# Kernel tuning notes

Hardware: AMD Instinct MI355X
Metric: run time of the kernel (lower is better)

Reference implementation:

```python
import jax, jax.numpy as jnp
import numpy as np

B, T, C = 2, 2048, 2048
N_HEAD, N_KV = 16, 2
D_HEAD = C // N_HEAD          # 128
R = N_HEAD // N_KV            # q heads per kv head = 8


def setup_inputs() -> dict:
    key = jax.random.key(0)
    ks = jax.random.split(key, 5)
    s = 0.02
    return {
        "x": jax.random.normal(ks[0], (B, T, C), dtype=jnp.float32),
        "Wq": jax.random.normal(ks[1], (C, C), dtype=jnp.float32) * s,
        "Wk": jax.random.normal(ks[2], (C, N_KV * D_HEAD), dtype=jnp.float32) * s,
        "Wv": jax.random.normal(ks[3], (C, N_KV * D_HEAD), dtype=jnp.float32) * s,
        "Wo": jax.random.normal(ks[4], (C, C), dtype=jnp.float32) * s,
    }


def reference(x, Wq, Wk, Wv, Wo):
    b, t, c = x.shape
    # projections (no bias per config.bias=False)
    q = (x @ Wq).reshape(b, t, N_KV, R, D_HEAD)        # group q heads by kv group
    k = (x @ Wk).reshape(b, t, N_KV, D_HEAD)
    v = (x @ Wv).reshape(b, t, N_KV, D_HEAD)
    scale = 1.0 / jnp.sqrt(jnp.float32(D_HEAD))
    # scores: [b, g(kv), r, tq, tk] -- broadcast kv heads instead of repeat_interleave
    att = jnp.einsum('btgrd,bsgd->bgrts', q, k) * scale
    causal = jnp.tril(jnp.ones((t, t), dtype=bool))
    att = jnp.where(causal, att, -jnp.inf)
    att = jax.nn.softmax(att, axis=-1)
    y = jnp.einsum('bgrts,bsgd->btgrd', att, v).reshape(b, t, c)
    return y @ Wo
```

## Files before the change

kernel.cpp:

```cpp
#include <hip/hip_runtime.h>
#include <stdint.h>

using bf16x8 = __attribute__((ext_vector_type(8))) __bf16;
using f32x4  = __attribute__((ext_vector_type(4))) float;

#define GLL(g, l) __builtin_amdgcn_global_load_lds(                                  \
    (const __attribute__((address_space(1))) void*)(g),                              \
    (__attribute__((address_space(3))) void*)(l), 16, 0, 0)

__device__ __forceinline__ unsigned short f2bf(float f) {
  unsigned u = __builtin_bit_cast(unsigned, f);
  u += 0x7FFF + ((u >> 16) & 1);
  return (unsigned short)(u >> 16);
}

__global__ __launch_bounds__(256) void cast_kernel(const float* __restrict__ in,
                                                   unsigned short* __restrict__ out, int n4) {
  int i = blockIdx.x * 256 + threadIdx.x;
  if (i >= n4) return;
  float4 v = reinterpret_cast<const float4*>(in)[i];
  ushort4 o;
  o.x = f2bf(v.x); o.y = f2bf(v.y); o.z = f2bf(v.z); o.w = f2bf(v.w);
  reinterpret_cast<ushort4*>(out)[i] = o;
}

__global__ __launch_bounds__(256) void tcast_kernel(const float* __restrict__ W,
                                                    unsigned short* __restrict__ Wt,
                                                    int K, int N) {
  __shared__ float T[64][65];
  const int k0 = blockIdx.x * 64, n0 = blockIdx.y * 64;
  const int t = threadIdx.x;
  const int r4 = t >> 6, c = t & 63;
#pragma unroll
  for (int p = 0; p < 16; ++p) {
    int r = p * 4 + r4;
    T[r][c] = W[(size_t)(k0 + r) * N + n0 + c];
  }
  __syncthreads();
#pragma unroll
  for (int p = 0; p < 16; ++p) {
    int r = p * 4 + r4;
    Wt[(size_t)(n0 + r) * K + k0 + c] = f2bf(T[c][r]);
  }
}

__global__ __launch_bounds__(256) void tv_kernel(const unsigned short* __restrict__ V,
                                                 unsigned short* __restrict__ Vt) {
  __shared__ unsigned short T[64][68];
  const int t0 = blockIdx.x * 64;
  const int d0 = blockIdx.y * 64;
  const int t = threadIdx.x;
  const int r4 = t >> 6, c = t & 63;
#pragma unroll
  for (int p = 0; p < 16; ++p) {
    int r = p * 4 + r4;
    T[r][c] = V[(size_t)(t0 + r) * 2560 + 2304 + d0 + c];
  }
  __syncthreads();
  const int b = t0 >> 11;
  const int tl = t0 & 2047;
#pragma unroll
  for (int p = 0; p < 16; ++p) {
    int dr = p * 4 + r4;
    int dg = d0 + dr;
    int g = dg >> 7, dl = dg & 127;
    Vt[(size_t)((b * 2 + g) * 128 + dl) * 2048 + tl + c] = T[c][dr];
  }
}

template <bool FP32OUT>
__global__ __launch_bounds__(256) void gemm_bt_kernel(const unsigned short* __restrict__ A,
                                                      const unsigned short* __restrict__ Bt,
                                                      void* __restrict__ Cout,
                                                      int K, int lda, int ldb, int ldc,
                                                      float scale, int nscale) {
  __shared__ __align__(16) unsigned short As[128 * 64];
  __shared__ __align__(16) unsigned short Bs[128 * 64];
  const int m0 = blockIdx.x * 128, n0 = blockIdx.y * 128;
  const int t = threadIdx.x;
  const int w = t >> 6, lane = t & 63;
  const int l15 = lane & 15, quad = lane >> 4;
  const int wm = (w >> 1) * 64, wn = (w & 1) * 64;

  const int srow = lane >> 3;
  const int sgl = (lane & 7) ^ srow;

  f32x4 acc[4][4] = {};

  for (int k0 = 0; k0 < K; k0 += 64) {
    __syncthreads();
#pragma unroll
    for (int p = 0; p < 4; ++p) {
      int rowbase = p * 32 + w * 8;
      GLL(&A[(size_t)(m0 + rowbase + srow) * lda + k0 + sgl * 8], &As[rowbase * 64]);
      GLL(&Bt[(size_t)(n0 + rowbase + srow) * ldb + k0 + sgl * 8], &Bs[rowbase * 64]);
    }
    __syncthreads();
#pragma unroll
    for (int kk = 0; kk < 64; kk += 32) {
      const int kg = kk >> 3;
      const int phys = ((kg + quad) ^ (l15 & 7)) * 8;
      bf16x8 af[4], bfr[4];
#pragma unroll
      for (int mt = 0; mt < 4; ++mt)
        af[mt] = *reinterpret_cast<const bf16x8*>(&As[(wm + mt * 16 + l15) * 64 + phys]);
#pragma unroll
      for (int nt = 0; nt < 4; ++nt)
        bfr[nt] = *reinterpret_cast<const bf16x8*>(&Bs[(wn + nt * 16 + l15) * 64 + phys]);
#pragma unroll
      for (int mt = 0; mt < 4; ++mt)
#pragma unroll
        for (int nt = 0; nt < 4; ++nt)
          acc[mt][nt] = __builtin_amdgcn_mfma_f32_16x16x32_bf16(af[mt], bfr[nt], acc[mt][nt], 0, 0, 0);
    }
  }

  const float sc = (n0 < nscale) ? scale : 1.0f;
#pragma unroll
  for (int mt = 0; mt < 4; ++mt) {
#pragma unroll
    for (int reg = 0; reg < 4; ++reg) {
      int row = m0 + wm + mt * 16 + quad * 4 + reg;
#pragma unroll
      for (int nt = 0; nt < 4; ++nt) {
        int col = n0 + wn + nt * 16 + l15;
        float v = acc[mt][nt][reg] * sc;
        if (FP32OUT)
          reinterpret_cast<float*>(Cout)[(size_t)row * ldc + col] = v;
        else
          reinterpret_cast<unsigned short*>(Cout)[(size_t)row * ldc + col] = f2bf(v);
      }
    }
  }
}

#define LDQK 2560
__global__ __launch_bounds__(256) void attn_kernel(const unsigned short* __restrict__ Q,
                                                   const unsigned short* __restrict__ Kg,
                                                   const unsigned short* __restrict__ Vt,
                                                   unsigned short* __restrict__ Y) {
  __shared__ __align__(16) unsigned short Ks[64 * 128];
  __shared__ __align__(16) unsigned short Vs[128 * 64];
  __shared__ __align__(16) unsigned short Ps[4][32 * 68];

  const int iq = blockIdx.x;
  const int hh = blockIdx.y & 15;
  const int b  = blockIdx.y >> 4;
  const int g  = hh >> 3;
  const int t = threadIdx.x;
  const int w = t >> 6, lane = t & 63;
  const int l15 = lane & 15, quad = lane >> 4;

  bf16x8 qf[2][4];
#pragma unroll
  for (int mi = 0; mi < 2; ++mi) {
    int qrow = iq * 128 + w * 32 + mi * 16 + l15;
    const unsigned short* qp = &Q[(size_t)(b * 2048 + qrow) * LDQK + hh * 128 + quad * 8];
#pragma unroll
    for (int dk = 0; dk < 4; ++dk)
      qf[mi][dk] = *reinterpret_cast<const bf16x8*>(qp + dk * 32);
  }

  f32x4 o[2][8] = {};
  float l_run[2][4] = {};

  const int k_r = lane >> 4;
  const int v_r = lane >> 3;

  const int nkt = 2 * iq + 2;
  for (int kt = 0; kt < nkt; ++kt) {
    __syncthreads();
#pragma unroll
    for (int p = 0; p < 4; ++p) {
      int rowbase = p * 16 + w * 4;
      int row = rowbase + k_r;
      int gl = (lane & 15) ^ (row & 15);
      GLL(&Kg[(size_t)(b * 2048 + kt * 64 + row) * LDQK + g * 128 + gl * 8], &Ks[rowbase * 128]);
    }
#pragma unroll
    for (int p = 0; p < 4; ++p) {
      int rowbase = p * 32 + w * 8;
      int row = rowbase + v_r;
      int gl = (lane & 7) ^ (row & 7);
      GLL(&Vt[(size_t)((b * 2 + g) * 128 + row) * 2048 + kt * 64 + gl * 8], &Vs[rowbase * 64]);
    }
    __syncthreads();

#pragma unroll
    for (int mi = 0; mi < 2; ++mi) {
      f32x4 s[4];
#pragma unroll
      for (int nt = 0; nt < 4; ++nt) {
        f32x4 a = {};
#pragma unroll
        for (int dk = 0; dk < 4; ++dk) {
          int phys = (dk * 4 + quad) ^ l15;
          bf16x8 kf = *reinterpret_cast<const bf16x8*>(&Ks[(nt * 16 + l15) * 128 + phys * 8]);
          a = __builtin_amdgcn_mfma_f32_16x16x32_bf16(qf[mi][dk], kf, a, 0, 0, 0);
        }
        s[nt] = a;
      }
      if (kt >= 2 * iq) {
#pragma unroll
        for (int nt = 0; nt < 4; ++nt) {
          int kcol = kt * 64 + nt * 16 + l15;
#pragma unroll
          for (int reg = 0; reg < 4; ++reg) {
            int qr = iq * 128 + w * 32 + mi * 16 + quad * 4 + reg;
            if (kcol > qr) s[nt][reg] = -1e30f;
          }
        }
      }
#pragma unroll
      for (int nt = 0; nt < 4; ++nt) {
#pragma unroll
        for (int reg = 0; reg < 4; ++reg) {
          float p = __builtin_exp2f(__builtin_fmaf(s[nt][reg], 1.44269504f, -23.08312064f));
          l_run[mi][reg] += p;
          Ps[w][(mi * 16 + quad * 4 + reg) * 68 + nt * 16 + l15] = f2bf(p);
        }
      }
    }

#pragma unroll
    for (int kk = 0; kk < 2; ++kk) {
      const int kg = kk * 4;
      bf16x8 pf[2];
#pragma unroll
      for (int mi = 0; mi < 2; ++mi)
        pf[mi] = *reinterpret_cast<const bf16x8*>(&Ps[w][(mi * 16 + l15) * 68 + kk * 32 + quad * 8]);
#pragma unroll
      for (int dt = 0; dt < 8; ++dt) {
        int phys = (kg + quad) ^ (l15 & 7);
        bf16x8 vf = *reinterpret_cast<const bf16x8*>(&Vs[(dt * 16 + l15) * 64 + phys * 8]);
#pragma unroll
        for (int mi = 0; mi < 2; ++mi)
          o[mi][dt] = __builtin_amdgcn_mfma_f32_16x16x32_bf16(pf[mi], vf, o[mi][dt], 0, 0, 0);
      }
    }
  }

#pragma unroll
  for (int off = 1; off <= 8; off <<= 1)
#pragma unroll
    for (int mi = 0; mi < 2; ++mi)
#pragma unroll
      for (int reg = 0; reg < 4; ++reg)
        l_run[mi][reg] += __shfl_xor(l_run[mi][reg], off);
  float inv[2][4];
#pragma unroll
  for (int mi = 0; mi < 2; ++mi)
#pragma unroll
    for (int reg = 0; reg < 4; ++reg) inv[mi][reg] = 1.0f / l_run[mi][reg];

#pragma unroll
  for (int mi = 0; mi < 2; ++mi)
#pragma unroll
    for (int dt = 0; dt < 8; ++dt)
#pragma unroll
      for (int reg = 0; reg < 4; ++reg) {
        int row = b * 2048 + iq * 128 + w * 32 + mi * 16 + quad * 4 + reg;
        int col = hh * 128 + dt * 16 + l15;
        Y[(size_t)row * 2048 + col] = f2bf(o[mi][dt][reg] * inv[mi][reg]);
      }
}

extern "C" void kernel_launch(void* const* d_in, const int* in_sizes, int n_in,
                              void* d_out, int out_size, void* d_ws, size_t ws_size,
                              hipStream_t stream) {
  const float* x  = (const float*)d_in[0];
  const float* Wq = (const float*)d_in[1];
  const float* Wk = (const float*)d_in[2];
  const float* Wv = (const float*)d_in[3];
  const float* Wo = (const float*)d_in[4];

  char* ws = (char*)d_ws;
  unsigned short* xb    = (unsigned short*)(ws + 0);
  unsigned short* Wqkvt = (unsigned short*)(ws + 16777216);
  unsigned short* Wot   = (unsigned short*)(ws + 27262976);
  unsigned short* QKVb  = (unsigned short*)(ws + 35651584);
  unsigned short* Vtb   = (unsigned short*)(ws + 56623104);
  unsigned short* Yb    = xb;

  cast_kernel<<<8192, 256, 0, stream>>>(x, xb, 2097152);
  tcast_kernel<<<dim3(32, 32), 256, 0, stream>>>(Wq, Wqkvt, 2048, 2048);
  tcast_kernel<<<dim3(32, 4),  256, 0, stream>>>(Wk, Wqkvt + (size_t)2048 * 2048, 2048, 256);
  tcast_kernel<<<dim3(32, 4),  256, 0, stream>>>(Wv, Wqkvt + (size_t)2304 * 2048, 2048, 256);
  tcast_kernel<<<dim3(32, 32), 256, 0, stream>>>(Wo, Wot, 2048, 2048);

  const float qscale = 0.08838834764831845f;
  gemm_bt_kernel<false><<<dim3(32, 20), 256, 0, stream>>>(xb, Wqkvt, QKVb,
                                                          2048, 2048, 2048, 2560, qscale, 2048);
  tv_kernel<<<dim3(64, 4), 256, 0, stream>>>(QKVb, Vtb);
  attn_kernel<<<dim3(16, 32), 256, 0, stream>>>(QKVb, QKVb + 2048, Vtb, Yb);
  gemm_bt_kernel<true><<<dim3(32, 16), 256, 0, stream>>>(Yb, Wot, d_out,
                                                         2048, 2048, 2048, 2048, 1.0f, 0);
}
```

Before: 324.5 us.

## Pair causal query tiles per block and prefetch K/V via registers

Each attention block now processes two query tiles (iq and 15-iq) to balance causal work, halving the grid. K/V tiles are prefetched one iteration ahead into registers and then stored to LDS, replacing direct global-to-LDS loads. The QK^T loop computes both row groups together to reuse K fragments. This trades lower occupancy (one block per CU, higher register use) for balanced work and overlapped loads.

After: 354.4 us. +9.2%, slower.

```diff
diff --git a/kernel.cpp b/kernel.cpp
--- a/kernel.cpp
+++ b/kernel.cpp
@@ -135,15 +135,15 @@
 }
 
 #define LDQK 2560
-__global__ __launch_bounds__(256) void attn_kernel(const unsigned short* __restrict__ Q,
-                                                   const unsigned short* __restrict__ Kg,
-                                                   const unsigned short* __restrict__ Vt,
-                                                   unsigned short* __restrict__ Y) {
+__global__ __launch_bounds__(256, 1) void attn_kernel(const unsigned short* __restrict__ Q,
+                                                      const unsigned short* __restrict__ Kg,
+                                                      const unsigned short* __restrict__ Vt,
+                                                      unsigned short* __restrict__ Y) {
   __shared__ __align__(16) unsigned short Ks[64 * 128];
   __shared__ __align__(16) unsigned short Vs[128 * 64];
   __shared__ __align__(16) unsigned short Ps[4][32 * 68];
 
-  const int iq = blockIdx.x;
+  const int bx = blockIdx.x;
   const int hh = blockIdx.y & 15;
   const int b  = blockIdx.y >> 4;
   const int g  = hh >> 3;
@@ -151,118 +151,141 @@
   const int w = t >> 6, lane = t & 63;
   const int l15 = lane & 15, quad = lane >> 4;
 
-  bf16x8 qf[2][4];
-#pragma unroll
-  for (int mi = 0; mi < 2; ++mi) {
-    int qrow = iq * 128 + w * 32 + mi * 16 + l15;
-    const unsigned short* qp = &Q[(size_t)(b * 2048 + qrow) * LDQK + hh * 128 + quad * 8];
-#pragma unroll
-    for (int dk = 0; dk < 4; ++dk)
-      qf[mi][dk] = *reinterpret_cast<const bf16x8*>(qp + dk * 32);
-  }
-
-  f32x4 o[2][8] = {};
-  float l_run[2][4] = {};
-
-  const int k_r = lane >> 4;
-  const int v_r = lane >> 3;
-
-  const int nkt = 2 * iq + 2;
-  for (int kt = 0; kt < nkt; ++kt) {
-    __syncthreads();
-#pragma unroll
-    for (int p = 0; p < 4; ++p) {
-      int rowbase = p * 16 + w * 4;
-      int row = rowbase + k_r;
-      int gl = (lane & 15) ^ (row & 15);
-      GLL(&Kg[(size_t)(b * 2048 + kt * 64 + row) * LDQK + g * 128 + gl * 8], &Ks[rowbase * 128]);
-    }
-#pragma unroll
-    for (int p = 0; p < 4; ++p) {
-      int rowbase = p * 32 + w * 8;
-      int row = rowbase + v_r;
-      int gl = (lane & 7) ^ (row & 7);
-      GLL(&Vt[(size_t)((b * 2 + g) * 128 + row) * 2048 + kt * 64 + gl * 8], &Vs[rowbase * 64]);
-    }
-    __syncthreads();
-
+  const unsigned short* Kbase = Kg + (size_t)b * 2048 * LDQK + g * 128;
+  const unsigned short* Vbase = Vt + (size_t)(b * 2 + g) * 128 * 2048;
+
+  const int krow = t >> 4;
+  const int kgl  = (t & 15);
+  const int vrow = t >> 3;
+  const int vgl  = (t & 7);
+
+  int4 kst[4], vst[4];
+#pragma unroll
+  for (int p = 0; p < 4; ++p) {
+    int rk = p * 16 + krow;
+    kst[p] = *reinterpret_cast<const int4*>(&Kbase[(size_t)rk * LDQK + ((kgl ^ (rk & 15)) * 8)]);
+    int rv = p * 32 + vrow;
+    vst[p] = *reinterpret_cast<const int4*>(&Vbase[(size_t)rv * 2048 + ((vgl ^ (rv & 7)) * 8)]);
+  }
+
+  for (int ph = 0; ph < 2; ++ph) {
+    const int iq = ph ? (15 - bx) : bx;
+
+    bf16x8 qf[2][4];
 #pragma unroll
     for (int mi = 0; mi < 2; ++mi) {
-      f32x4 s[4];
+      int qrow = iq * 128 + w * 32 + mi * 16 + l15;
+      const unsigned short* qp = &Q[(size_t)(b * 2048 + qrow) * LDQK + hh * 128 + quad * 8];
+#pragma unroll
+      for (int dk = 0; dk < 4; ++dk)
+        qf[mi][dk] = *reinterpret_cast<const bf16x8*>(qp + dk * 32);
+    }
+
+    f32x4 o[2][8] = {};
+    float l_run[2][4] = {};
+    const int nkt = 2 * iq + 2;
+
+    for (int kt = 0; kt < nkt; ++kt) {
+      __syncthreads();
+#pragma unroll
+      for (int p = 0; p < 4; ++p) {
+        int rk = p * 16 + krow;
+        *reinterpret_cast<int4*>(&Ks[rk * 128 + kgl * 8]) = kst[p];
+        int rv = p * 32 + vrow;
+        *reinterpret_cast<int4*>(&Vs[rv * 64 + vgl * 8]) = vst[p];
+      }
+      const bool have_next = (kt + 1 < nkt) || (ph == 0);
+      const int ktn = (kt + 1 < nkt) ? (kt + 1) : 0;
+      if (have_next) {
+        const unsigned short* kb = Kbase + (size_t)(ktn * 64) * LDQK;
+        const unsigned short* vb = Vbase + ktn * 64;
+#pragma unroll
+        for (int p = 0; p < 4; ++p) {
+          int rk = p * 16 + krow;
+          kst[p] = *reinterpret_cast<const int4*>(&kb[(size_t)rk * LDQK + ((kgl ^ (rk & 15)) * 8)]);
+          int rv = p * 32 + vrow;
+          vst[p] = *reinterpret_cast<const int4*>(&vb[(size_t)rv * 2048 + ((vgl ^ (rv & 7)) * 8)]);
+        }
+      }
+      __syncthreads();
+
+      f32x4 s[2][4] = {};
 #pragma unroll
       for (int nt = 0; nt < 4; ++nt) {
-        f32x4 a = {};
 #pragma unroll
         for (int dk = 0; dk < 4; ++dk) {
           int phys = (dk * 4 + quad) ^ l15;
           bf16x8 kf = *reinterpret_cast<const bf16x8*>(&Ks[(nt * 16 + l15) * 128 + phys * 8]);
-          a = __builtin_amdgcn_mfma_f32_16x16x32_bf16(qf[mi][dk], kf, a, 0, 0, 0);
+          s[0][nt] = __builtin_amdgcn_mfma_f32_16x16x32_bf16(qf[0][dk], kf, s[0][nt], 0, 0, 0);
+          s[1][nt] = __builtin_amdgcn_mfma_f32_16x16x32_bf16(qf[1][dk], kf, s[1][nt], 0, 0, 0);
         }
-        s[nt] = a;
       }
       if (kt >= 2 * iq) {
 #pragma unroll
-        for (int nt = 0; nt < 4; ++nt) {
-          int kcol = kt * 64 + nt * 16 + l15;
+        for (int mi = 0; mi < 2; ++mi)
+#pragma unroll
+          for (int nt = 0; nt < 4; ++nt) {
+            int kcol = kt * 64 + nt * 16 + l15;
+#pragma unroll
+            for (int reg = 0; reg < 4; ++reg) {
+              int qr = iq * 128 + w * 32 + mi * 16 + quad * 4 + reg;
+              if (kcol > qr) s[mi][nt][reg] = -1e30f;
+            }
+          }
+      }
+#pragma unroll
+      for (int mi = 0; mi < 2; ++mi)
+#pragma unroll
+        for (int nt = 0; nt < 4; ++nt)
 #pragma unroll
           for (int reg = 0; reg < 4; ++reg) {
-            int qr = iq * 128 + w * 32 + mi * 16 + quad * 4 + reg;
-            if (kcol > qr) s[nt][reg] = -1e30f;
+            float p = __builtin_exp2f(__builtin_fmaf(s[mi][nt][reg], 1.44269504f, -23.08312064f));
+            l_run[mi][reg] += p;
+            Ps[w][(mi * 16 + quad * 4 + reg) * 68 + nt * 16 + l15] = f2bf(p);
           }
+
+#pragma unroll
+      for (int kk = 0; kk < 2; ++kk) {
+        const int kg = kk * 4;
+        bf16x8 pf[2];
+#pragma unroll
+        for (int mi = 0; mi < 2; ++mi)
+          pf[mi] = *reinterpret_cast<const bf16x8*>(&Ps[w][(mi * 16 + l15) * 68 + kk * 32 + quad * 8]);
+#pragma unroll
+        for (int dt = 0; dt < 8; ++dt) {
+          int phys = (kg + quad) ^ (l15 & 7);
+          bf16x8 vf = *reinterpret_cast<const bf16x8*>(&Vs[(dt * 16 + l15) * 64 + phys * 8]);
+#pragma unroll
+          for (int mi = 0; mi < 2; ++mi)
+            o[mi][dt] = __builtin_amdgcn_mfma_f32_16x16x32_bf16(pf[mi], vf, o[mi][dt], 0, 0, 0);
         }
       }
-#pragma unroll
-      for (int nt = 0; nt < 4; ++nt) {
+    }
+
+#pragma unroll
+    for (int off = 1; off <= 8; off <<= 1)
+#pragma unroll
+      for (int mi = 0; mi < 2; ++mi)
+#pragma unroll
+        for (int reg = 0; reg < 4; ++reg)
+          l_run[mi][reg] += __shfl_xor(l_run[mi][reg], off);
+    float inv[2][4];
+#pragma unroll
+    for (int mi = 0; mi < 2; ++mi)
+#pragma unroll
+      for (int reg = 0; reg < 4; ++reg) inv[mi][reg] = 1.0f / l_run[mi][reg];
+
+#pragma unroll
+    for (int mi = 0; mi < 2; ++mi)
+#pragma unroll
+      for (int dt = 0; dt < 8; ++dt)
 #pragma unroll
         for (int reg = 0; reg < 4; ++reg) {
-          float p = __builtin_exp2f(__builtin_fmaf(s[nt][reg], 1.44269504f, -23.08312064f));
-          l_run[mi][reg] += p;
-          Ps[w][(mi * 16 + quad * 4 + reg) * 68 + nt * 16 + l15] = f2bf(p);
+          int row = b * 2048 + iq * 128 + w * 32 + mi * 16 + quad * 4 + reg;
+          int col = hh * 128 + dt * 16 + l15;
+          Y[(size_t)row * 2048 + col] = f2bf(o[mi][dt][reg] * inv[mi][reg]);
         }
-      }
-    }
-
-#pragma unroll
-    for (int kk = 0; kk < 2; ++kk) {
-      const int kg = kk * 4;
-      bf16x8 pf[2];
-#pragma unroll
-      for (int mi = 0; mi < 2; ++mi)
-        pf[mi] = *reinterpret_cast<const bf16x8*>(&Ps[w][(mi * 16 + l15) * 68 + kk * 32 + quad * 8]);
-#pragma unroll
-      for (int dt = 0; dt < 8; ++dt) {
-        int phys = (kg + quad) ^ (l15 & 7);
-        bf16x8 vf = *reinterpret_cast<const bf16x8*>(&Vs[(dt * 16 + l15) * 64 + phys * 8]);
-#pragma unroll
-        for (int mi = 0; mi < 2; ++mi)
-          o[mi][dt] = __builtin_amdgcn_mfma_f32_16x16x32_bf16(pf[mi], vf, o[mi][dt], 0, 0, 0);
-      }
-    }
-  }
-
-#pragma unroll
-  for (int off = 1; off <= 8; off <<= 1)
-#pragma unroll
-    for (int mi = 0; mi < 2; ++mi)
-#pragma unroll
-      for (int reg = 0; reg < 4; ++reg)
-        l_run[mi][reg] += __shfl_xor(l_run[mi][reg], off);
-  float inv[2][4];
-#pragma unroll
-  for (int mi = 0; mi < 2; ++mi)
-#pragma unroll
-    for (int reg = 0; reg < 4; ++reg) inv[mi][reg] = 1.0f / l_run[mi][reg];
-
-#pragma unroll
-  for (int mi = 0; mi < 2; ++mi)
-#pragma unroll
-    for (int dt = 0; dt < 8; ++dt)
-#pragma unroll
-      for (int reg = 0; reg < 4; ++reg) {
-        int row = b * 2048 + iq * 128 + w * 32 + mi * 16 + quad * 4 + reg;
-        int col = hh * 128 + dt * 16 + l15;
-        Y[(size_t)row * 2048 + col] = f2bf(o[mi][dt][reg] * inv[mi][reg]);
-      }
+  }
 }
 
 extern "C" void kernel_launch(void* const* d_in, const int* in_sizes, int n_in,
@@ -292,7 +315,7 @@
   gemm_bt_kernel<false><<<dim3(32, 20), 256, 0, stream>>>(xb, Wqkvt, QKVb,
                                                           2048, 2048, 2048, 2560, qscale, 2048);
   tv_kernel<<<dim3(64, 4), 256, 0, stream>>>(QKVb, Vtb);
-  attn_kernel<<<dim3(16, 32), 256, 0, stream>>>(QKVb, QKVb + 2048, Vtb, Yb);
+  attn_kernel<<<dim3(8, 32), 256, 0, stream>>>(QKVb, QKVb + 2048, Vtb, Yb);
   gemm_bt_kernel<true><<<dim3(32, 16), 256, 0, stream>>>(Yb, Wot, d_out,
                                                          2048, 2048, 2048, 2048, 1.0f, 0);
 }
```

## Split attention KV range in two, pair causal query tiles, double-buffer K/V

Applied to the files above, without the earlier changes.

Each attention block now handles two query tiles (iq and 15-iq) to balance causal work, and the KV tiles are split into even/odd halves across two blocks. Each half writes partial unnormalized outputs and row sums, and a new merge kernel adds them and normalizes. K/V tiles are double-buffered with async global-to-LDS loads so the next tile's fetch overlaps compute. Partial outputs use d_out as fp32 scratch plus a bf16 buffer, which adds an extra memory pass and rounds one half to bf16 before the merge.

After: 286.7 us. -11.6%, faster.

```diff
diff --git a/kernel.cpp b/kernel.cpp
--- a/kernel.cpp
+++ b/kernel.cpp
@@ -12,6 +12,10 @@
   unsigned u = __builtin_bit_cast(unsigned, f);
   u += 0x7FFF + ((u >> 16) & 1);
   return (unsigned short)(u >> 16);
+}
+__device__ __forceinline__ float bf2f(unsigned short u) {
+  unsigned v = ((unsigned)u) << 16;
+  return __builtin_bit_cast(float, v);
 }
 
 __global__ __launch_bounds__(256) void cast_kernel(const float* __restrict__ in,
@@ -135,134 +139,191 @@
 }
 
 #define LDQK 2560
-__global__ __launch_bounds__(256) void attn_kernel(const unsigned short* __restrict__ Q,
-                                                   const unsigned short* __restrict__ Kg,
-                                                   const unsigned short* __restrict__ Vt,
-                                                   unsigned short* __restrict__ Y) {
-  __shared__ __align__(16) unsigned short Ks[64 * 128];
-  __shared__ __align__(16) unsigned short Vs[128 * 64];
-  __shared__ __align__(16) unsigned short Ps[4][32 * 68];
-
-  const int iq = blockIdx.x;
-  const int hh = blockIdx.y & 15;
-  const int b  = blockIdx.y >> 4;
+__global__ __launch_bounds__(256, 2) void attn_kernel(const unsigned short* __restrict__ Q,
+                                                      const unsigned short* __restrict__ Kg,
+                                                      const unsigned short* __restrict__ Vt,
+                                                      float* __restrict__ O0,
+                                                      unsigned short* __restrict__ O1,
+                                                      float* __restrict__ L) {
+  __shared__ __align__(16) unsigned short Ks[2][64 * 128];
+  __shared__ __align__(16) unsigned short Vs[2][128 * 64];
+  __shared__ __align__(16) unsigned short Pw[4][32 * 32];
+
+  const int s  = blockIdx.x;
+  const int bx = blockIdx.y;
+  const int hh = blockIdx.z & 15;
+  const int b  = blockIdx.z >> 4;
   const int g  = hh >> 3;
-  const int t = threadIdx.x;
-  const int w = t >> 6, lane = t & 63;
+  const int t  = threadIdx.x;
+  const int wg = t >> 6, lane = t & 63;
   const int l15 = lane & 15, quad = lane >> 4;
 
-  bf16x8 qf[2][4];
-#pragma unroll
-  for (int mi = 0; mi < 2; ++mi) {
-    int qrow = iq * 128 + w * 32 + mi * 16 + l15;
-    const unsigned short* qp = &Q[(size_t)(b * 2048 + qrow) * LDQK + hh * 128 + quad * 8];
-#pragma unroll
-    for (int dk = 0; dk < 4; ++dk)
-      qf[mi][dk] = *reinterpret_cast<const bf16x8*>(qp + dk * 32);
-  }
-
-  f32x4 o[2][8] = {};
-  float l_run[2][4] = {};
+  const unsigned short* Kbase = Kg + (size_t)b * 2048 * LDQK + g * 128;
+  const unsigned short* Vbase = Vt + (size_t)(b * 2 + g) * 128 * 2048;
 
   const int k_r = lane >> 4;
   const int v_r = lane >> 3;
 
-  const int nkt = 2 * iq + 2;
-  for (int kt = 0; kt < nkt; ++kt) {
-    __syncthreads();
+  auto issueK = [&](int tile, unsigned short* dst) {
+    const unsigned short* kb = Kbase + (size_t)(tile * 64) * LDQK;
 #pragma unroll
     for (int p = 0; p < 4; ++p) {
-      int rowbase = p * 16 + w * 4;
+      int rowbase = p * 16 + wg * 4;
       int row = rowbase + k_r;
       int gl = (lane & 15) ^ (row & 15);
-      GLL(&Kg[(size_t)(b * 2048 + kt * 64 + row) * LDQK + g * 128 + gl * 8], &Ks[rowbase * 128]);
-    }
+      GLL(&kb[(size_t)row * LDQK + gl * 8], &dst[rowbase * 128]);
+    }
+  };
+  auto issueV = [&](int tile, unsigned short* dst) {
+    const unsigned short* vb = Vbase + tile * 64;
 #pragma unroll
     for (int p = 0; p < 4; ++p) {
-      int rowbase = p * 32 + w * 8;
+      int rowbase = p * 32 + wg * 8;
       int row = rowbase + v_r;
       int gl = (lane & 7) ^ (row & 7);
-      GLL(&Vt[(size_t)((b * 2 + g) * 128 + row) * 2048 + kt * 64 + gl * 8], &Vs[rowbase * 64]);
-    }
-    __syncthreads();
-
+      GLL(&vb[(size_t)row * 2048 + gl * 8], &dst[rowbase * 64]);
+    }
+  };
+
+  int pb = 0;
+  issueK(s, Ks[0]);
+  issueV(s, Vs[0]);
+
+  for (int ph = 0; ph < 2; ++ph) {
+    const int iq = ph ? (15 - bx) : bx;
+
+    bf16x8 qf[2][4];
 #pragma unroll
     for (int mi = 0; mi < 2; ++mi) {
-      f32x4 s[4];
+      int qrow = iq * 128 + wg * 32 + mi * 16 + l15;
+      const unsigned short* qp = &Q[(size_t)(b * 2048 + qrow) * LDQK + hh * 128 + quad * 8];
+#pragma unroll
+      for (int dk = 0; dk < 4; ++dk)
+        qf[mi][dk] = *reinterpret_cast<const bf16x8*>(qp + dk * 32);
+    }
+
+    f32x4 o[2][8] = {};
+    float l_run[2][4] = {};
+
+    for (int j = 0; j <= iq; ++j) {
+      const int tile = 2 * j + s;
+      __syncthreads();
+      const int cur = pb, nxt = pb ^ 1;
+
+      if (j < iq) {
+        issueK(tile + 2, Ks[nxt]);
+        issueV(tile + 2, Vs[nxt]);
+      } else if (ph == 0) {
+        issueK(s, Ks[nxt]);
+        issueV(s, Vs[nxt]);
+      }
+
+      f32x4 sc[2][4] = {};
 #pragma unroll
       for (int nt = 0; nt < 4; ++nt) {
-        f32x4 a = {};
 #pragma unroll
         for (int dk = 0; dk < 4; ++dk) {
           int phys = (dk * 4 + quad) ^ l15;
-          bf16x8 kf = *reinterpret_cast<const bf16x8*>(&Ks[(nt * 16 + l15) * 128 + phys * 8]);
-          a = __builtin_amdgcn_mfma_f32_16x16x32_bf16(qf[mi][dk], kf, a, 0, 0, 0);
-        }
-        s[nt] = a;
-      }
-      if (kt >= 2 * iq) {
-#pragma unroll
-        for (int nt = 0; nt < 4; ++nt) {
-          int kcol = kt * 64 + nt * 16 + l15;
-#pragma unroll
-          for (int reg = 0; reg < 4; ++reg) {
-            int qr = iq * 128 + w * 32 + mi * 16 + quad * 4 + reg;
-            if (kcol > qr) s[nt][reg] = -1e30f;
+          bf16x8 kf = *reinterpret_cast<const bf16x8*>(&Ks[cur][(nt * 16 + l15) * 128 + phys * 8]);
+          sc[0][nt] = __builtin_amdgcn_mfma_f32_16x16x32_bf16(qf[0][dk], kf, sc[0][nt], 0, 0, 0);
+          sc[1][nt] = __builtin_amdgcn_mfma_f32_16x16x32_bf16(qf[1][dk], kf, sc[1][nt], 0, 0, 0);
+        }
+      }
+      if (j == iq) {
+#pragma unroll
+        for (int mi = 0; mi < 2; ++mi)
+#pragma unroll
+          for (int nt = 0; nt < 4; ++nt) {
+            int kcol = tile * 64 + nt * 16 + l15;
+#pragma unroll
+            for (int reg = 0; reg < 4; ++reg) {
+              int qr = iq * 128 + wg * 32 + mi * 16 + quad * 4 + reg;
+              if (kcol > qr) sc[mi][nt][reg] = -1e30f;
+            }
           }
-        }
-      }
-#pragma unroll
-      for (int nt = 0; nt < 4; ++nt) {
-#pragma unroll
-        for (int reg = 0; reg < 4; ++reg) {
-          float p = __builtin_exp2f(__builtin_fmaf(s[nt][reg], 1.44269504f, -23.08312064f));
-          l_run[mi][reg] += p;
-          Ps[w][(mi * 16 + quad * 4 + reg) * 68 + nt * 16 + l15] = f2bf(p);
-        }
-      }
-    }
-
-#pragma unroll
-    for (int kk = 0; kk < 2; ++kk) {
-      const int kg = kk * 4;
-      bf16x8 pf[2];
+      }
+
+#pragma unroll
+      for (int kk = 0; kk < 2; ++kk) {
+#pragma unroll
+        for (int ntl = 0; ntl < 2; ++ntl) {
+          const int nt = kk * 2 + ntl;
+#pragma unroll
+          for (int mi = 0; mi < 2; ++mi)
+#pragma unroll
+            for (int reg = 0; reg < 4; ++reg) {
+              float p = __builtin_exp2f(__builtin_fmaf(sc[mi][nt][reg], 1.44269504f, -23.08312064f));
+              l_run[mi][reg] += p;
+              int row = mi * 16 + quad * 4 + reg;
+              int slot = (ntl * 2 + (l15 >> 3)) ^ (row & 3);
+              Pw[wg][row * 32 + slot * 8 + (l15 & 7)] = f2bf(p);
+            }
+        }
+        bf16x8 pf[2];
+#pragma unroll
+        for (int mi = 0; mi < 2; ++mi) {
+          int row = mi * 16 + l15;
+          int slot = quad ^ (row & 3);
+          pf[mi] = *reinterpret_cast<const bf16x8*>(&Pw[wg][row * 32 + slot * 8]);
+        }
+#pragma unroll
+        for (int dt = 0; dt < 8; ++dt) {
+          int phys = ((kk * 4 + quad) ^ (l15 & 7));
+          bf16x8 vf = *reinterpret_cast<const bf16x8*>(&Vs[cur][(dt * 16 + l15) * 64 + phys * 8]);
+#pragma unroll
+          for (int mi = 0; mi < 2; ++mi)
+            o[mi][dt] = __builtin_amdgcn_mfma_f32_16x16x32_bf16(pf[mi], vf, o[mi][dt], 0, 0, 0);
+        }
+      }
+      pb ^= 1;
+    }
+
+#pragma unroll
+    for (int off = 1; off <= 8; off <<= 1)
 #pragma unroll
       for (int mi = 0; mi < 2; ++mi)
-        pf[mi] = *reinterpret_cast<const bf16x8*>(&Ps[w][(mi * 16 + l15) * 68 + kk * 32 + quad * 8]);
-#pragma unroll
-      for (int dt = 0; dt < 8; ++dt) {
-        int phys = (kg + quad) ^ (l15 & 7);
-        bf16x8 vf = *reinterpret_cast<const bf16x8*>(&Vs[(dt * 16 + l15) * 64 + phys * 8]);
-#pragma unroll
-        for (int mi = 0; mi < 2; ++mi)
-          o[mi][dt] = __builtin_amdgcn_mfma_f32_16x16x32_bf16(pf[mi], vf, o[mi][dt], 0, 0, 0);
-      }
-    }
-  }
-
-#pragma unroll
-  for (int off = 1; off <= 8; off <<= 1)
+#pragma unroll
+        for (int reg = 0; reg < 4; ++reg)
+          l_run[mi][reg] += __shfl_xor(l_run[mi][reg], off);
+
 #pragma unroll
     for (int mi = 0; mi < 2; ++mi)
 #pragma unroll
-      for (int reg = 0; reg < 4; ++reg)
-        l_run[mi][reg] += __shfl_xor(l_run[mi][reg], off);
-  float inv[2][4];
-#pragma unroll
-  for (int mi = 0; mi < 2; ++mi)
-#pragma unroll
-    for (int reg = 0; reg < 4; ++reg) inv[mi][reg] = 1.0f / l_run[mi][reg];
-
-#pragma unroll
-  for (int mi = 0; mi < 2; ++mi)
-#pragma unroll
-    for (int dt = 0; dt < 8; ++dt)
-#pragma unroll
       for (int reg = 0; reg < 4; ++reg) {
-        int row = b * 2048 + iq * 128 + w * 32 + mi * 16 + quad * 4 + reg;
-        int col = hh * 128 + dt * 16 + l15;
-        Y[(size_t)row * 2048 + col] = f2bf(o[mi][dt][reg] * inv[mi][reg]);
-      }
+        int row = wg * 32 + mi * 16 + quad * 4 + reg;
+        size_t base = (size_t)(b * 2048 + iq * 128 + row) * 2048 + hh * 128;
+        if (s == 0) {
+#pragma unroll
+          for (int dt = 0; dt < 8; ++dt)
+            O0[base + dt * 16 + l15] = o[mi][dt][reg];
+        } else {
+#pragma unroll
+          for (int dt = 0; dt < 8; ++dt)
+            O1[base + dt * 16 + l15] = f2bf(o[mi][dt][reg]);
+        }
+        if (l15 == 0)
+          L[(size_t)s * 65536 + (size_t)(b * 2048 + iq * 128 + row) * 16 + hh] = l_run[mi][reg];
+      }
+  }
+}
+
+__global__ __launch_bounds__(256) void merge_kernel(const float* __restrict__ O0,
+                                                    unsigned short* __restrict__ O1,
+                                                    const float* __restrict__ L) {
+  int i4 = blockIdx.x * 256 + threadIdx.x;
+  int e = i4 << 2;
+  int tr = e >> 11;
+  int hh = (e >> 7) & 15;
+  float l = L[tr * 16 + hh] + L[65536 + tr * 16 + hh];
+  float inv = 1.0f / l;
+  float4 a = reinterpret_cast<const float4*>(O0)[i4];
+  ushort4 u = reinterpret_cast<const ushort4*>(O1)[i4];
+  ushort4 r;
+  r.x = f2bf((a.x + bf2f(u.x)) * inv);
+  r.y = f2bf((a.y + bf2f(u.y)) * inv);
+  r.z = f2bf((a.z + bf2f(u.z)) * inv);
+  r.w = f2bf((a.w + bf2f(u.w)) * inv);
+  reinterpret_cast<ushort4*>(O1)[i4] = r;
 }
 
 extern "C" void kernel_launch(void* const* d_in, const int* in_sizes, int n_in,
@@ -280,6 +341,7 @@
   unsigned short* Wot   = (unsigned short*)(ws + 27262976);
   unsigned short* QKVb  = (unsigned short*)(ws + 35651584);
   unsigned short* Vtb   = (unsigned short*)(ws + 56623104);
+  float*          Lb    = (float*)(ws + 58720256);
   unsigned short* Yb    = xb;
 
   cast_kernel<<<8192, 256, 0, stream>>>(x, xb, 2097152);
@@ -292,7 +354,9 @@
   gemm_bt_kernel<false><<<dim3(32, 20), 256, 0, stream>>>(xb, Wqkvt, QKVb,
                                                           2048, 2048, 2048, 2560, qscale, 2048);
   tv_kernel<<<dim3(64, 4), 256, 0, stream>>>(QKVb, Vtb);
-  attn_kernel<<<dim3(16, 32), 256, 0, stream>>>(QKVb, QKVb + 2048, Vtb, Yb);
+  attn_kernel<<<dim3(2, 8, 32), 256, 0, stream>>>(QKVb, QKVb + 2048, Vtb,
+                                                  (float*)d_out, Yb, Lb);
+  merge_kernel<<<8192, 256, 0, stream>>>((const float*)d_out, Yb, Lb);
   gemm_bt_kernel<true><<<dim3(32, 16), 256, 0, stream>>>(Yb, Wot, d_out,
                                                          2048, 2048, 2048, 2048, 1.0f, 0);
 }
```
